# Kernel tuning notes

Measured on AMD Instinct MI355X. Metric: run time of the kernel, lower is better.

Reference implementation:

```python
import jax, jax.numpy as jnp
import numpy as np

B, L, H, TE = 256, 2048, 64, 64  # batch, seq len, hidden_size, num_time_enc_dims


def _lin_init(k, out_d, in_d):
    bound = 1.0 / np.sqrt(in_d)
    kw, kb = jax.random.split(k)
    w = jax.random.uniform(kw, (out_d, in_d), jnp.float32, -bound, bound)
    b = jax.random.uniform(kb, (out_d,), jnp.float32, -bound, bound)
    return w, b


def setup_inputs() -> dict:
    key = jax.random.key(0)
    ks = jax.random.split(key, 16)
    x_xy = jax.random.normal(ks[0], (B, L, 2), jnp.float32)
    mask = jax.random.bernoulli(ks[1], 0.8, (B, L, 1)).astype(jnp.float32)  # 0 => masked position
    x = jnp.concatenate([x_xy, mask], axis=-1)  # (B,L,3)
    t = jax.random.uniform(ks[2], (B, L, 1), jnp.float32)
    te_w1, te_b1 = _lin_init(ks[3], TE, 1)
    te_w2, te_b2 = _lin_init(ks[4], TE, TE)
    fproj_w, fproj_b = _lin_init(ks[5], H, 3 + TE)
    bproj_w, bproj_b = _lin_init(ks[6], H, 3 + TE)
    fwz, fbz = _lin_init(ks[7], H, H)
    fwh, fbh = _lin_init(ks[8], H, H)
    bwz, bbz = _lin_init(ks[9], H, H)
    bwh, bbh = _lin_init(ks[10], H, H)
    head_hidden = max((2 * H + TE) // 2, 128)  # = 128
    gh_w1, gh_b1 = _lin_init(ks[11], head_hidden, 2 * H + TE)
    gh_w2, gh_b2 = _lin_init(ks[12], 1, head_hidden)
    mask_token = jnp.array([0.0, 0.01], jnp.float32) + jnp.array([0.1, 0.001], jnp.float32) * jax.random.normal(ks[13], (2,), jnp.float32)
    return dict(x=x, t=t, mask_token=mask_token,
                te_w1=te_w1, te_b1=te_b1, te_w2=te_w2, te_b2=te_b2,
                fproj_w=fproj_w, fproj_b=fproj_b, bproj_w=bproj_w, bproj_b=bproj_b,
                fwz=fwz, fbz=fbz, fwh=fwh, fbh=fbh,
                bwz=bwz, bbz=bbz, bwh=bwh, bbh=bbh,
                gh_w1=gh_w1, gh_b1=gh_b1, gh_w2=gh_w2, gh_b2=gh_b2)


def _mingru_prestates(inp, wz, bz, wh, bh, reverse):
    # inp: (B,L,H). Returns the hidden state BEFORE each step's update, in
    # time order, matching the torch code which stores h_* before cell.step.
    z = jax.nn.sigmoid(jnp.einsum('blh,oh->blo', inp, wz) + bz)
    h_tilde = jnp.tanh(jnp.einsum('blh,oh->blo', inp, wh) + bh)

    def step(h, zh):
        z_t, ht_t = zh
        return (1.0 - z_t) * h + z_t * ht_t, h  # emit pre-update carry

    h0 = jnp.zeros((inp.shape[0], wz.shape[0]), inp.dtype)
    _, hs = jax.lax.scan(step, h0,
                         (jnp.swapaxes(z, 0, 1), jnp.swapaxes(h_tilde, 0, 1)),
                         reverse=reverse)
    return jnp.swapaxes(hs, 0, 1)  # (B,L,H)


def reference(x, t, mask_token,
              te_w1, te_b1, te_w2, te_b2,
              fproj_w, fproj_b, bproj_w, bproj_b,
              fwz, fbz, fwh, fbh,
              bwz, bbz, bwh, bbh,
              gh_w1, gh_b1, gh_w2, gh_b2):
    mask_chan = x[..., 2:3]                      # (B,L,1)
    masked_pos = mask_chan == 0
    x_first2 = jnp.where(masked_pos, mask_token.reshape(1, 1, 2), x[..., :2])
    x3 = jnp.concatenate([x_first2, mask_chan], axis=-1)  # (B,L,3)

    t_enc = jax.nn.relu(jnp.einsum('blk,ok->blo', t, te_w1) + te_b1)
    t_enc = jnp.einsum('blk,ok->blo', t_enc, te_w2) + te_b2  # (B,L,TE)

    x_cat = jnp.concatenate([x3, t_enc], axis=-1)  # (B,L,3+TE)

    inp_fwd = jnp.einsum('blk,ok->blo', x_cat, fproj_w) + fproj_b
    inp_bwd = jnp.einsum('blk,ok->blo', x_cat, bproj_w) + bproj_b

    h_fwd = _mingru_prestates(inp_fwd, fwz, fbz, fwh, fbh, reverse=False)  # state after steps 0..t-1
    h_bwd = _mingru_prestates(inp_bwd, bwz, bbz, bwh, bbh, reverse=True)   # state after steps L-1..t+1

    h_fwd_final = h_fwd[:, -1:, :]  # state after steps 0..L-2
    h_bwd_final = h_bwd[:, 0:1, :]  # state after steps L-1..1

    unmasked = mask_chan > 0
    h_fwd_apply = jnp.where(unmasked, h_fwd, h_fwd_final)
    h_bwd_apply = jnp.where(unmasked, h_bwd, h_bwd_final)

    h_bi = jnp.concatenate([h_fwd_apply, h_bwd_apply, t_enc], axis=-1)  # (B,L,2H+TE)
    hid = jax.nn.relu(jnp.einsum('blk,ok->blo', h_bi, gh_w1) + gh_b1)
    preds = jnp.einsum('blk,ok->blo', hid, gh_w2) + gh_b2  # (B,L,1)
    return preds
```

## Files before the change

### kernel.cpp

```cpp
#include <hip/hip_runtime.h>
#include <stdint.h>

#define NB 256
#define NL 2048

typedef __attribute__((ext_vector_type(8))) short short8;
typedef __attribute__((ext_vector_type(4))) float f32x4;
#define MFMA16(a,b,c) __builtin_amdgcn_mfma_f32_16x16x32_bf16(a,b,c,0,0,0)

static __device__ __forceinline__ unsigned short f2bf(float f) {
    union { float f; uint32_t u; } v; v.f = f;
    uint32_t u = v.u;
    uint32_t r = u + 0x7fffu + ((u >> 16) & 1u);
    return (unsigned short)(r >> 16);
}
static __device__ __forceinline__ float bflo(uint32_t u) {
    union { uint32_t u; float f; } v; v.u = u << 16; return v.f;
}
static __device__ __forceinline__ float bfhi(uint32_t u) {
    union { uint32_t u; float f; } v; v.u = u & 0xffff0000u; return v.f;
}
#if __has_builtin(__builtin_amdgcn_cvt_pk_bf16_f32)
typedef __attribute__((ext_vector_type(2))) __bf16 bf16x2_t;
static __device__ __forceinline__ uint32_t pk2(float lo, float hi) {
    union { bf16x2_t v; uint32_t u; } c;
    c.v = __builtin_amdgcn_cvt_pk_bf16_f32(lo, hi);
    return c.u;
}
static __device__ __forceinline__ unsigned short bf1(float v) {
    union { bf16x2_t v; uint32_t u; } c;
    c.v = __builtin_amdgcn_cvt_pk_bf16_f32(v, v);
    return (unsigned short)(c.u & 0xffffu);
}
#else
static __device__ __forceinline__ uint32_t pk2(float lo, float hi) {
    return ((uint32_t)f2bf(hi) << 16) | (uint32_t)f2bf(lo);
}
static __device__ __forceinline__ unsigned short bf1(float v) { return f2bf(v); }
#endif
static __device__ __forceinline__ short8 frag8(const float* p) {
    short8 r;
#pragma unroll
    for (int j = 0; j < 8; ++j) r[j] = (short)f2bf(p[j]);
    return r;
}

__global__ __launch_bounds__(256, 3) void prep_kernel(
    const float* __restrict__ x, const float* __restrict__ t,
    const float* __restrict__ mtok,
    const float* __restrict__ te_w1, const float* __restrict__ te_b1,
    const float* __restrict__ te_w2, const float* __restrict__ te_b2,
    const float* __restrict__ fpw, const float* __restrict__ fpb,
    const float* __restrict__ bpw, const float* __restrict__ bpb,
    const float* __restrict__ fwz, const float* __restrict__ fbz,
    const float* __restrict__ fwh, const float* __restrict__ fbh,
    const float* __restrict__ bwz, const float* __restrict__ bbz,
    const float* __restrict__ bwh, const float* __restrict__ bbh,
    int b0,
    uint32_t* __restrict__ abf,
    uint32_t* __restrict__ abb)
{
    __shared__ __align__(16) unsigned short s_te1[64*72];
    __shared__ __align__(16) unsigned short s_tenc[64*72];
    __shared__ __align__(16) unsigned short s_xa[64*40];
    __shared__ __align__(16) unsigned short s_inp[2][64*72];

    const int tid = threadIdx.x;
    const int w   = tid >> 6;
    const int l   = tid & 63;
    const int lq  = l >> 4;
    const int ln  = l & 15;

    short8 bte[2];
    {
        const float* row = te_w2 + (w*16 + ln)*64;
#pragma unroll
        for (int ks = 0; ks < 2; ++ks) bte[ks] = frag8(row + lq*8 + ks*32);
    }
    short8 bpj[2][3];
#pragma unroll
    for (int p = 0; p < 2; ++p) {
        const int g = 2*w + p;
        const float* PW = (g < 4) ? fpw : bpw;
        const float* row = PW + ((g & 3)*16 + ln)*67;
#pragma unroll
        for (int ks = 0; ks < 2; ++ks) {
            float tmp[8];
#pragma unroll
            for (int j = 0; j < 8; ++j) tmp[j] = row[3 + lq*8 + ks*32 + j];
            bpj[p][ks] = frag8(tmp);
        }
        {
            float tmp[8];
#pragma unroll
            for (int j = 0; j < 8; ++j) tmp[j] = (lq == 0 && j < 3) ? row[j] : 0.f;
            bpj[p][2] = frag8(tmp);
        }
    }
    const int wdir = w >> 1, wnp = w & 1;
    short8 bgz[2][2], bgh[2][2];
    float bias_gz[2], bias_gh[2];
    {
        const float* WZ = wdir ? bwz : fwz;
        const float* WH = wdir ? bwh : fwh;
        const float* BZ = wdir ? bbz : fbz;
        const float* BH = wdir ? bbh : fbh;
#pragma unroll
        for (int nt2 = 0; nt2 < 2; ++nt2) {
            const int nt = wnp*2 + nt2;
            const float* rz = WZ + (nt*16 + ln)*64;
            const float* rh = WH + (nt*16 + ln)*64;
#pragma unroll
            for (int ks = 0; ks < 2; ++ks) {
                bgz[nt2][ks] = frag8(rz + lq*8 + ks*32);
                bgh[nt2][ks] = frag8(rh + lq*8 + ks*32);
            }
            bias_gz[nt2] = BZ[nt*16 + ln];
            bias_gh[nt2] = BH[nt*16 + ln];
        }
    }
    const float bias_te = te_b2[w*16 + ln];
    float bias_pj[2];
#pragma unroll
    for (int p = 0; p < 2; ++p) {
        const int g = 2*w + p;
        bias_pj[p] = ((g < 4) ? fpb : bpb)[(g & 3)*16 + ln];
    }
    const float mt0 = mtok[0], mt1 = mtok[1];

    const int baseposl = blockIdx.x * 256;

    auto P0 = [&](int ch) {
        const int gbase = (b0 << 11) + baseposl + ch*64;
        const int pos = tid & 63;
        const float tv = t[gbase + pos];
        const int k0 = (tid >> 6) * 16;
        uint32_t* dst = (uint32_t*)(s_te1 + pos*72 + k0);
#pragma unroll
        for (int kk = 0; kk < 16; kk += 2) {
            float v0 = fmaxf(fmaf(tv, te_w1[k0+kk],   te_b1[k0+kk]),   0.f);
            float v1 = fmaxf(fmaf(tv, te_w1[k0+kk+1], te_b1[k0+kk+1]), 0.f);
            dst[kk >> 1] = pk2(v0, v1);
        }
        if (tid < 64) {
            const float* xp = x + (size_t)(gbase + tid)*3;
            const float mc = xp[2];
            const float x0 = (mc == 0.f) ? mt0 : xp[0];
            const float x1 = (mc == 0.f) ? mt1 : xp[1];
            uint32_t* xr = (uint32_t*)(s_xa + tid*40);
            xr[0] = pk2(x0, x1);
            xr[1] = pk2(mc, 0.f);
        }
    };
    auto G1 = [&]() {
        const int o = w*16 + ln;
#pragma unroll
        for (int mt = 0; mt < 4; ++mt) {
            f32x4 c = {0.f, 0.f, 0.f, 0.f};
#pragma unroll
            for (int ks = 0; ks < 2; ++ks) {
                const short8 a = *(const short8*)(s_te1 + (mt*16+ln)*72 + lq*8 + ks*32);
                c = MFMA16(a, bte[ks], c);
            }
#pragma unroll
            for (int r = 0; r < 4; ++r) {
                const int m = mt*16 + lq*4 + r;
                s_tenc[m*72 + o] = bf1(c[r] + bias_te);
            }
        }
    };
    auto G2 = [&]() {
#pragma unroll
        for (int mt = 0; mt < 4; ++mt) {
            short8 a0 = *(const short8*)(s_tenc + (mt*16+ln)*72 + lq*8);
            short8 a1 = *(const short8*)(s_tenc + (mt*16+ln)*72 + lq*8 + 32);
            short8 a2 = *(const short8*)(s_xa   + (mt*16+ln)*40 + lq*8);
#pragma unroll
            for (int p = 0; p < 2; ++p) {
                const int g = 2*w + p;
                const int dir = g >> 2;
                const int o = (g & 3)*16 + ln;
                f32x4 c = {0.f, 0.f, 0.f, 0.f};
                c = MFMA16(a0, bpj[p][0], c);
                c = MFMA16(a1, bpj[p][1], c);
                c = MFMA16(a2, bpj[p][2], c);
#pragma unroll
                for (int r = 0; r < 4; ++r) {
                    const int m = mt*16 + lq*4 + r;
                    s_inp[dir][m*72 + o] = bf1(c[r] + bias_pj[p]);
                }
            }
        }
    };
    auto G3 = [&](int ch) {
        const int chbase = baseposl + ch*64;
        const int ll0 = chbase & 2047;
        const int bl  = chbase >> 11;
        uint32_t* abD = (wdir ? abb : abf) + (size_t)(bl*64)*NL + ll0;
#pragma unroll
        for (int mt = 0; mt < 4; ++mt) {
            const short8 a0 = *(const short8*)(s_inp[wdir] + (mt*16+ln)*72 + lq*8);
            const short8 a1 = *(const short8*)(s_inp[wdir] + (mt*16+ln)*72 + lq*8 + 32);
#pragma unroll
            for (int nt2 = 0; nt2 < 2; ++nt2) {
                f32x4 cz = {0.f, 0.f, 0.f, 0.f};
                f32x4 ch2 = {0.f, 0.f, 0.f, 0.f};
                cz  = MFMA16(a0, bgz[nt2][0], cz);
                cz  = MFMA16(a1, bgz[nt2][1], cz);
                ch2 = MFMA16(a0, bgh[nt2][0], ch2);
                ch2 = MFMA16(a1, bgh[nt2][1], ch2);
                const int o = (wnp*2 + nt2)*16 + ln;
                uint4 v;
                uint32_t* vp = (uint32_t*)&v;
#pragma unroll
                for (int r = 0; r < 4; ++r) {
                    const float az = cz[r]  + bias_gz[nt2];
                    const float ah = ch2[r] + bias_gh[nt2];
                    const float z  = __builtin_amdgcn_rcpf(1.f + __expf(-az));
                    const float cc = fminf(fmaxf(ah, -15.f), 15.f);
                    const float e2 = __expf(2.f * cc);
                    const float th = 1.f - 2.f * __builtin_amdgcn_rcpf(e2 + 1.f);
                    vp[r] = pk2(1.f - z, z * th);
                }
                *(uint4*)(abD + (size_t)o*NL + mt*16 + lq*4) = v;
            }
        }
    };

#pragma unroll
    for (int i = tid; i < 64*20; i += 256) {
        if ((i % 20) >= 2) ((uint32_t*)s_xa)[i] = 0;
    }
    P0(0);
    __syncthreads();
    G1();
    __syncthreads();
    G2();
    __syncthreads();
#pragma unroll 1
    for (int ch = 0; ch < 4; ++ch) {
        G3(ch);
        if (ch < 3) P0(ch + 1);
        __syncthreads();
        if (ch < 3) {
            G1();
            __syncthreads();
            G2();
            __syncthreads();
        }
    }
}

#define SSTR 129

__global__ __launch_bounds__(256) void scan3_kernel(
    const uint32_t* __restrict__ abf, const uint32_t* __restrict__ abb,
    unsigned short* __restrict__ hf, unsigned short* __restrict__ hb)
{
    __shared__ uint32_t s_seg[32*SSTR];
    __shared__ float s_A[8][33], s_B[8][33], s_Hin[8][33];
    __shared__ float s_H[32];

    const int rl  = blockIdx.x >> 2;
    const int dir = (blockIdx.x >> 1) & 1;
    const int h0  = (blockIdx.x & 1) * 32;
    const int tid = threadIdx.x;
    const int h   = tid & 31;
    const int q   = tid >> 5;

    const uint32_t* ab = (dir ? abb : abf) + (size_t)rl * 64 * NL + (size_t)h0 * NL;
    unsigned short* out = (dir ? hb : hf) + (size_t)rl * NL * 64 + h0;

    if (tid < 32) s_H[tid] = 0.f;
    __syncthreads();

#pragma unroll 1
    for (int si = 0; si < 16; ++si) {
        const int s  = dir ? (15 - si) : si;
        const int l0 = s * 128;

#pragma unroll
        for (int rep = 0; rep < 16; ++rep) {
            const int idx = rep*256 + tid;
            const int hh = idx >> 7, xx = idx & 127;
            s_seg[hh*SSTR + xx] = ab[(size_t)hh*NL + l0 + xx];
        }
        __syncthreads();

        uint32_t regs[16];
        float A = 1.f, Bc = 0.f;
#pragma unroll
        for (int i = 0; i < 16; ++i) {
            const int g = q*16 + i;
            const int xx = dir ? (127 - g) : g;
            const uint32_t uab = s_seg[h*SSTR + xx];
            regs[i] = uab;
            Bc = fmaf(bflo(uab), Bc, bfhi(uab));
            A *= bflo(uab);
        }
        s_A[q][h] = A; s_B[q][h] = Bc;
        __syncthreads();

        if (tid < 32) {
            float H = s_H[tid];
#pragma unroll
            for (int qq = 0; qq < 8; ++qq) {
                s_Hin[qq][tid] = H;
                H = fmaf(s_A[qq][tid], H, s_B[qq][tid]);
            }
            s_H[tid] = H;
        }
        __syncthreads();

        float hv = s_Hin[q][h];
#pragma unroll
        for (int i = 0; i < 16; ++i) {
            const int g = q*16 + i;
            const int xx = dir ? (127 - g) : g;
            const uint32_t uab = regs[i];
            out[(size_t)(l0 + xx)*64 + h] = bf1(hv);
            hv = fmaf(bflo(uab), hv, bfhi(uab));
        }
        __syncthreads();
    }
}

__global__ __launch_bounds__(256, 3) void head_kernel(
    const float* __restrict__ x, const float* __restrict__ t,
    const float* __restrict__ te_w1, const float* __restrict__ te_b1,
    const float* __restrict__ te_w2, const float* __restrict__ te_b2,
    const unsigned short* __restrict__ hf, const unsigned short* __restrict__ hb,
    const float* __restrict__ w1, const float* __restrict__ b1,
    const float* __restrict__ w2, const float* __restrict__ b2,
    int b0,
    float* __restrict__ out)
{
    __shared__ __align__(16) unsigned short s_a[64*200];
    __shared__ __align__(16) unsigned short s_te1[64*72];
    __shared__ float s_part[4][64];
    __shared__ float s_mc[64];

    const int tid = threadIdx.x;
    const int w   = tid >> 6;
    const int l   = tid & 63;
    const int lq  = l >> 4;
    const int ln  = l & 15;

    short8 bw1[2][6];
    float b1v[2], w2v[2];
#pragma unroll
    for (int p = 0; p < 2; ++p) {
        const int o = (2*w + p)*16 + ln;
        const float* row = w1 + o*192;
#pragma unroll
        for (int ks = 0; ks < 6; ++ks) bw1[p][ks] = frag8(row + lq*8 + ks*32);
        b1v[p] = b1[o];
        w2v[p] = w2[o];
    }
    short8 bte[2];
    {
        const float* row = te_w2 + (w*16 + ln)*64;
#pragma unroll
        for (int ks = 0; ks < 2; ++ks) bte[ks] = frag8(row + lq*8 + ks*32);
    }
    const float bias_te = te_b2[w*16 + ln];
    const float bias2 = b2[0];

    const int baseposl = blockIdx.x * 256;

    auto A = [&](int ch) {
        const int gbase = (b0 << 11) + baseposl + ch*64;
        if (tid < 64) s_mc[tid] = x[(size_t)(gbase + tid)*3 + 2];
        const int pos = tid & 63;
        const float tv = t[gbase + pos];
        const int k0 = (tid >> 6) * 16;
        uint32_t* dst = (uint32_t*)(s_te1 + pos*72 + k0);
#pragma unroll
        for (int kk = 0; kk < 16; kk += 2) {
            float v0 = fmaxf(fmaf(tv, te_w1[k0+kk],   te_b1[k0+kk]),   0.f);
            float v1 = fmaxf(fmaf(tv, te_w1[k0+kk+1], te_b1[k0+kk+1]), 0.f);
            dst[kk >> 1] = pk2(v0, v1);
        }
    };
    auto Bp = [&](int ch) {
        const int chbase = baseposl + ch*64;
        const int ll0 = chbase & 2047;
        const int bl  = chbase >> 11;
        const size_t rowbase = (size_t)bl * NL * 64;
#pragma unroll
        for (int rep = 0; rep < 4; ++rep) {
            const int idx = rep*256 + tid;
            const int seg = idx >> 9;
            const int row = (idx >> 3) & 63;
            const int c   = idx & 7;
            const bool unm = s_mc[row] > 0.f;
            const uint4* src = (seg == 0)
                ? (const uint4*)(hf + rowbase + (size_t)(unm ? (ll0+row) : (NL-1))*64)
                : (const uint4*)(hb + rowbase + (size_t)(unm ? (ll0+row) : 0)*64);
            ((uint4*)s_a)[row*25 + seg*8 + c] = src[c];
        }
        const int o = w*16 + ln;
#pragma unroll
        for (int mt = 0; mt < 4; ++mt) {
            f32x4 c = {0.f, 0.f, 0.f, 0.f};
#pragma unroll
            for (int ks = 0; ks < 2; ++ks) {
                const short8 a = *(const short8*)(s_te1 + (mt*16+ln)*72 + lq*8 + ks*32);
                c = MFMA16(a, bte[ks], c);
            }
#pragma unroll
            for (int r = 0; r < 4; ++r) {
                const int m = mt*16 + lq*4 + r;
                s_a[m*200 + 128 + o] = bf1(c[r] + bias_te);
            }
        }
    };
    auto Cp = [&]() {
#pragma unroll
        for (int mt = 0; mt < 4; ++mt) {
            short8 af[6];
#pragma unroll
            for (int ks = 0; ks < 6; ++ks)
                af[ks] = *(const short8*)(s_a + (mt*16+ln)*200 + lq*8 + ks*32);
            float vs[4] = {0.f, 0.f, 0.f, 0.f};
#pragma unroll
            for (int p = 0; p < 2; ++p) {
                f32x4 c = {0.f, 0.f, 0.f, 0.f};
#pragma unroll
                for (int ks = 0; ks < 6; ++ks) c = MFMA16(af[ks], bw1[p][ks], c);
#pragma unroll
                for (int r = 0; r < 4; ++r)
                    vs[r] += fmaxf(c[r] + b1v[p], 0.f) * w2v[p];
            }
#pragma unroll
            for (int mask = 1; mask < 16; mask <<= 1) {
#pragma unroll
                for (int r = 0; r < 4; ++r)
                    vs[r] += __shfl_xor(vs[r], mask);
            }
            if (ln == 0) {
#pragma unroll
                for (int r = 0; r < 4; ++r)
                    s_part[w][mt*16 + lq*4 + r] = vs[r];
            }
        }
    };
    auto Dp = [&](int ch) {
        const int gbase = (b0 << 11) + baseposl + ch*64;
        if (tid < 64) {
            out[gbase + tid] = s_part[0][tid] + s_part[1][tid]
                             + s_part[2][tid] + s_part[3][tid] + bias2;
        }
    };

    A(0);
    __syncthreads();
#pragma unroll 1
    for (int ch = 0; ch < 4; ++ch) {
        Bp(ch);
        __syncthreads();
        Cp();
        __syncthreads();
        Dp(ch);
        if (ch < 3) A(ch + 1);
        __syncthreads();
    }
}

extern "C" void kernel_launch(void* const* d_in, const int* in_sizes, int n_in,
                              void* d_out, int out_size, void* d_ws, size_t ws_size,
                              hipStream_t stream)
{
    const float* x     = (const float*)d_in[0];
    const float* t     = (const float*)d_in[1];
    const float* mtok  = (const float*)d_in[2];
    const float* te_w1 = (const float*)d_in[3];
    const float* te_b1 = (const float*)d_in[4];
    const float* te_w2 = (const float*)d_in[5];
    const float* te_b2 = (const float*)d_in[6];
    const float* fpw   = (const float*)d_in[7];
    const float* fpb   = (const float*)d_in[8];
    const float* bpw   = (const float*)d_in[9];
    const float* bpb   = (const float*)d_in[10];
    const float* fwz   = (const float*)d_in[11];
    const float* fbz   = (const float*)d_in[12];
    const float* fwh   = (const float*)d_in[13];
    const float* fbh   = (const float*)d_in[14];
    const float* bwz   = (const float*)d_in[15];
    const float* bbz   = (const float*)d_in[16];
    const float* bwh   = (const float*)d_in[17];
    const float* bbh   = (const float*)d_in[18];
    const float* w1    = (const float*)d_in[19];
    const float* b1    = (const float*)d_in[20];
    const float* w2    = (const float*)d_in[21];
    const float* b2    = (const float*)d_in[22];

    const size_t per_b = 1572864ull;
    int Bg = NB;
    while ((size_t)Bg * per_b > ws_size && Bg > 1) Bg >>= 1;
    const int nG = NB / Bg;

    char* ws = (char*)d_ws;
    uint32_t*       abf  = (uint32_t*)(ws);
    uint32_t*       abb  = abf + (size_t)Bg * 64 * NL;
    unsigned short* hf   = (unsigned short*)(abb + (size_t)Bg * 64 * NL);
    unsigned short* hb   = hf + (size_t)Bg * NL * 64;

    for (int g = 0; g < nG; ++g) {
        const int b0 = g * Bg;

        prep_kernel<<<8 * Bg, 256, 0, stream>>>(
            x, t, mtok, te_w1, te_b1, te_w2, te_b2,
            fpw, fpb, bpw, bpb, fwz, fbz, fwh, fbh, bwz, bbz, bwh, bbh,
            b0, abf, abb);

        scan3_kernel<<<4 * Bg, 256, 0, stream>>>(abf, abb, hf, hb);

        head_kernel<<<8 * Bg, 256, 0, stream>>>(
            x, t, te_w1, te_b1, te_w2, te_b2,
            hf, hb, w1, b1, w2, b2, b0, (float*)d_out);
    }
}
```

Baseline: 378.1 us.

## Store gate pairs time-major and use LDS-only barriers

Changes the intermediate (1-z, z*h~) buffer from [batch][hidden][time] to [batch][time][hidden]. The prep kernel now writes one scalar per element instead of a 16-byte vector per hidden row, and the scan kernel loads time-major rows, 32 hidden values per row. It also replaces __syncthreads with a barrier that only waits on LDS counters, so outstanding global stores need not drain at each barrier. The new layout gives scattered 4-byte stores in prep and shorter contiguous reads in scan. The weaker barrier depends on no global-memory ordering being needed between the stages.

```diff
diff --git a/kernel.cpp b/kernel.cpp
--- a/kernel.cpp
+++ b/kernel.cpp
@@ -43,6 +43,11 @@
 #pragma unroll
     for (int j = 0; j < 8; ++j) r[j] = (short)f2bf(p[j]);
     return r;
+}
+
+static __device__ __forceinline__ void barrier_lds() {
+    asm volatile("s_waitcnt lgkmcnt(0)" ::: "memory");
+    __builtin_amdgcn_s_barrier();
 }
 
 __global__ __launch_bounds__(256, 3) void prep_kernel(
@@ -196,7 +201,7 @@
         const int chbase = baseposl + ch*64;
         const int ll0 = chbase & 2047;
         const int bl  = chbase >> 11;
-        uint32_t* abD = (wdir ? abb : abf) + (size_t)(bl*64)*NL + ll0;
+        uint32_t* abD = (wdir ? abb : abf) + ((size_t)bl*NL + ll0)*64;
 #pragma unroll
         for (int mt = 0; mt < 4; ++mt) {
             const short8 a0 = *(const short8*)(s_inp[wdir] + (mt*16+ln)*72 + lq*8);
@@ -210,8 +215,6 @@
                 ch2 = MFMA16(a0, bgh[nt2][0], ch2);
                 ch2 = MFMA16(a1, bgh[nt2][1], ch2);
                 const int o = (wnp*2 + nt2)*16 + ln;
-                uint4 v;
-                uint32_t* vp = (uint32_t*)&v;
 #pragma unroll
                 for (int r = 0; r < 4; ++r) {
                     const float az = cz[r]  + bias_gz[nt2];
@@ -220,9 +223,8 @@
                     const float cc = fminf(fmaxf(ah, -15.f), 15.f);
                     const float e2 = __expf(2.f * cc);
                     const float th = 1.f - 2.f * __builtin_amdgcn_rcpf(e2 + 1.f);
-                    vp[r] = pk2(1.f - z, z * th);
+                    abD[(size_t)(mt*16 + lq*4 + r)*64 + o] = pk2(1.f - z, z * th);
                 }
-                *(uint4*)(abD + (size_t)o*NL + mt*16 + lq*4) = v;
             }
         }
     };
@@ -232,21 +234,21 @@
         if ((i % 20) >= 2) ((uint32_t*)s_xa)[i] = 0;
     }
     P0(0);
-    __syncthreads();
+    barrier_lds();
     G1();
-    __syncthreads();
+    barrier_lds();
     G2();
-    __syncthreads();
+    barrier_lds();
 #pragma unroll 1
     for (int ch = 0; ch < 4; ++ch) {
         G3(ch);
         if (ch < 3) P0(ch + 1);
-        __syncthreads();
+        barrier_lds();
         if (ch < 3) {
             G1();
-            __syncthreads();
+            barrier_lds();
             G2();
-            __syncthreads();
+            barrier_lds();
         }
     }
 }
@@ -268,11 +270,11 @@
     const int h   = tid & 31;
     const int q   = tid >> 5;
 
-    const uint32_t* ab = (dir ? abb : abf) + (size_t)rl * 64 * NL + (size_t)h0 * NL;
+    const uint32_t* ab = (dir ? abb : abf) + (size_t)rl * NL * 64 + h0;
     unsigned short* out = (dir ? hb : hf) + (size_t)rl * NL * 64 + h0;
 
     if (tid < 32) s_H[tid] = 0.f;
-    __syncthreads();
+    barrier_lds();
 
 #pragma unroll 1
     for (int si = 0; si < 16; ++si) {
@@ -282,10 +284,11 @@
 #pragma unroll
         for (int rep = 0; rep < 16; ++rep) {
             const int idx = rep*256 + tid;
-            const int hh = idx >> 7, xx = idx & 127;
-            s_seg[hh*SSTR + xx] = ab[(size_t)hh*NL + l0 + xx];
-        }
-        __syncthreads();
+            const int hh = idx & 31;
+            const int ll = idx >> 5;
+            s_seg[hh*SSTR + ll] = ab[(size_t)(l0 + ll)*64 + hh];
+        }
+        barrier_lds();
 
         uint32_t regs[16];
         float A = 1.f, Bc = 0.f;
@@ -299,7 +302,7 @@
             A *= bflo(uab);
         }
         s_A[q][h] = A; s_B[q][h] = Bc;
-        __syncthreads();
+        barrier_lds();
 
         if (tid < 32) {
             float H = s_H[tid];
@@ -310,7 +313,7 @@
             }
             s_H[tid] = H;
         }
-        __syncthreads();
+        barrier_lds();
 
         float hv = s_Hin[q][h];
 #pragma unroll
@@ -321,7 +324,7 @@
             out[(size_t)(l0 + xx)*64 + h] = bf1(hv);
             hv = fmaf(bflo(uab), hv, bfhi(uab));
         }
-        __syncthreads();
+        barrier_lds();
     }
 }
 
@@ -454,16 +457,16 @@
     };
 
     A(0);
-    __syncthreads();
+    barrier_lds();
 #pragma unroll 1
     for (int ch = 0; ch < 4; ++ch) {
         Bp(ch);
-        __syncthreads();
+        barrier_lds();
         Cp();
-        __syncthreads();
+        barrier_lds();
         Dp(ch);
         if (ch < 3) A(ch + 1);
-        __syncthreads();
+        barrier_lds();
     }
 }
 
```

Measured after the change: 370.9 us. Within noise of the previous version (-1.9%).
